# Performance work log

Hardware: AMD Instinct MI355X
Metric: run time of the kernel (lower is better)

Reference implementation:

```python
import jax, jax.numpy as jnp
import numpy as np

IN_FEATURES_LS = (8, 16, 32, 64, 128)
OUT_FEATURES = 512
MAX_FEAT = max(IN_FEATURES_LS)


def setup_inputs() -> dict:
    key = jax.random.key(0)
    k_x, k_idx, k_w, k_b = jax.random.split(key, 4)
    B, S = 16, 2048
    x = jax.random.normal(k_x, (B, S, MAX_FEAT), dtype=jnp.float32)
    # actual patch size per token: sample an index into in_features_ls
    idx = jax.random.randint(k_idx, (B, S), 0, len(IN_FEATURES_LS))
    in_feat_size = jnp.array(IN_FEATURES_LS, dtype=jnp.int64)[idx]
    weight = jax.random.normal(k_w, (len(IN_FEATURES_LS), OUT_FEATURES, MAX_FEAT), dtype=jnp.float32) * 0.05
    bias = jax.random.normal(k_b, (len(IN_FEATURES_LS), OUT_FEATURES), dtype=jnp.float32) * 0.05
    return {"x": x, "in_feat_size": in_feat_size, "weight": weight, "bias": bias}


def reference(x, in_feat_size, weight, bias):
    sizes = jnp.asarray(IN_FEATURES_LS)                       # [K]
    # mask padding columns of each expert's weight: [K, max_feat]
    feat_mask = (jnp.arange(MAX_FEAT)[None, :] < sizes[:, None]).astype(x.dtype)
    w = weight * feat_mask[:, None, :]                        # [K, out, max_feat]
    # all K projections computed unconditionally (faithful to original)
    y = jnp.einsum('bsi,koi->bsko', x, w) + bias              # [B, S, K, out]
    sel = (in_feat_size[..., None] == sizes).astype(x.dtype)  # [B, S, K] one-hot
    return jnp.einsum('bsko,bsk->bso', y, sel)                # [B, S, out]
```

## Files before the change

### kernel.cpp

```cpp
#include <hip/hip_runtime.h>

#define NEXP 5
#define MAXF 128
#define NOUT 512
#define NBMAX 256
#define PERMOFF (64 + NBMAX * NEXP)

typedef __attribute__((ext_vector_type(8))) short short8;
typedef __attribute__((ext_vector_type(4))) float floatx4;

__device__ __forceinline__ ushort f2bf(float f) {
    uint u = __float_as_uint(f);
    u += 0x7FFF + ((u >> 16) & 1);
    return (ushort)(u >> 16);
}


__global__ __launch_bounds__(256) void misl_prep(
    const int* __restrict__ feat, const float* __restrict__ w,
    int* __restrict__ ws, ushort* __restrict__ wb, int n, int nb) {
    if ((int)blockIdx.x < nb) {
        __shared__ int lcnt[NEXP];
        const int tid = threadIdx.x;
        if (tid < NEXP) lcnt[tid] = 0;
        __syncthreads();
        const int t = blockIdx.x * 256 + tid;
        if (t < n) { const int e = __ffs(feat[t]) - 4; atomicAdd(&lcnt[e], 1); }
        __syncthreads();
        if (tid < NEXP) ws[64 + blockIdx.x * NEXP + tid] = lcnt[tid];
    } else {
        const int idx = ((int)blockIdx.x - nb) * 256 + threadIdx.x;
        const int lane = idx & 63, nb16 = (idx >> 6) & 31;
        const int s = (idx >> 11) & 3, e = idx >> 13;
        if (e < NEXP) {
            const int ncol = nb16 * 16 + (lane & 15);
            const int k0 = s * 32 + (lane >> 4) * 8;
            const int K = 8 << e;
            const float* wr = w + ((size_t)e * NOUT + ncol) * MAXF + k0;
            short8 v;
            #pragma unroll
            for (int j = 0; j < 8; ++j)
                v[j] = (short)((k0 + j < K) ? f2bf(wr[j]) : (ushort)0);
            *(short8*)(wb + (size_t)idx * 8) = v;
        }
    }
}

__global__ __launch_bounds__(256) void misl_scatter(
    const int* __restrict__ feat, int* __restrict__ ws, int n, int nb) {
    __shared__ int ph[NBMAX * NEXP];
    __shared__ int lcnt[NEXP], lbase[NEXP], ltot[NEXP];
    const int tid = threadIdx.x;
    for (int i = tid; i < nb * NEXP; i += 256) ph[i] = ws[64 + i];
    if (tid < NEXP) lcnt[tid] = 0;
    __syncthreads();
    if (tid < NEXP) {
        int tot = 0, pre = 0;
        for (int bb = 0; bb < nb; ++bb) {
            if (bb == (int)blockIdx.x) pre = tot;
            tot += ph[bb * NEXP + tid];
        }
        ltot[tid] = tot; lbase[tid] = pre;
    }
    __syncthreads();
    if (tid < NEXP) {
        int seg = 0;
        for (int e = 0; e < tid; ++e) seg += ltot[e];
        lbase[tid] += seg;
        if (blockIdx.x == 0) { ws[tid] = ltot[tid]; ws[8 + tid] = seg; }
    }
    __syncthreads();
    const int t = blockIdx.x * 256 + tid;
    if (t < n) {
        const int e = __ffs(feat[t]) - 4;
        const int r = atomicAdd(&lcnt[e], 1);
        ws[PERMOFF + lbase[e] + r] = t;
    }
}

template <int NS>
__device__ __forceinline__ void mfma_group(
    const float* __restrict__ x, const ushort* __restrict__ wbe,
    const float* __restrict__ be, const int* __restrict__ ltok, int tcnt,
    int lane, int n_base, float* __restrict__ out) {
    const int m = lane & 15, q = lane >> 4;
    floatx4 acc[4];
    #pragma unroll
    for (int bi = 0; bi < 4; ++bi) {
        const float bv = be[n_base + bi * 16 + m];
        acc[bi] = floatx4{bv, bv, bv, bv};
    }
    const int tokA = ltok[m];
    const float* xr = x + (size_t)tokA * MAXF + q * 8;
    #pragma unroll
    for (int s = 0; s < NS; ++s) {
        const float4 xa = *(const float4*)(xr + s * 32);
        const float4 xb = *(const float4*)(xr + s * 32 + 4);
        short8 af;
        af[0] = (short)f2bf(xa.x); af[1] = (short)f2bf(xa.y);
        af[2] = (short)f2bf(xa.z); af[3] = (short)f2bf(xa.w);
        af[4] = (short)f2bf(xb.x); af[5] = (short)f2bf(xb.y);
        af[6] = (short)f2bf(xb.z); af[7] = (short)f2bf(xb.w);
        #pragma unroll
        for (int bi = 0; bi < 4; ++bi) {
            const short8 bf = *(const short8*)(
                wbe + ((size_t)(s * 32 + (n_base >> 4) + bi) * 64 + lane) * 8);
            acc[bi] = __builtin_amdgcn_mfma_f32_16x16x32_bf16(af, bf, acc[bi], 0, 0, 0);
        }
    }
    #pragma unroll
    for (int r = 0; r < 4; ++r) {
        const int mi = q * 4 + r;
        if (mi < tcnt) {
            const int tok = ltok[mi];
            float* orow = out + (size_t)tok * NOUT + n_base + m;
            #pragma unroll
            for (int bi = 0; bi < 4; ++bi) orow[bi * 16] = acc[bi][r];
        }
    }
}

__global__ __launch_bounds__(256) void misl_main(
    const float* __restrict__ x, const ushort* __restrict__ wb,
    const float* __restrict__ b, const int* __restrict__ ws,
    float* __restrict__ out) {
    const int g = blockIdx.x >> 1;
    const int half = blockIdx.x & 1;
    const int c[NEXP] = {ws[0], ws[1], ws[2], ws[3], ws[4]};
    const int sg[NEXP] = {ws[8], ws[9], ws[10], ws[11], ws[12]};

    int gb = 0, e = -1, lg = 0;
    #pragma unroll
    for (int j = 0; j < NEXP; ++j) {
        const int ee = 4 - j;
        const int ng = (c[ee] + 15) >> 4;
        if (e < 0 && g < gb + ng) { e = ee; lg = g - gb; }
        gb += ng;
    }
    if (e < 0) return;

    int tcnt = c[e] - lg * 16;
    if (tcnt > 16) tcnt = 16;

    __shared__ int ltok[16];
    if (threadIdx.x < 16) {
        const int ti = ((int)threadIdx.x < tcnt) ? (int)threadIdx.x : tcnt - 1;
        ltok[threadIdx.x] = ws[PERMOFF + sg[e] + lg * 16 + ti];
    }
    __syncthreads();

    const int lane = threadIdx.x & 63;
    const int wave = __builtin_amdgcn_readfirstlane(threadIdx.x >> 6);
    const int n_base = half * 256 + wave * 64;
    const ushort* wbe = wb + (size_t)e * 4 * 32 * 64 * 8;
    const float* be = b + e * NOUT;

    switch (e) {
        case 0: mfma_group<1>(x, wbe, be, ltok, tcnt, lane, n_base, out); break;
        case 1: mfma_group<1>(x, wbe, be, ltok, tcnt, lane, n_base, out); break;
        case 2: mfma_group<1>(x, wbe, be, ltok, tcnt, lane, n_base, out); break;
        case 3: mfma_group<2>(x, wbe, be, ltok, tcnt, lane, n_base, out); break;
        case 4: mfma_group<4>(x, wbe, be, ltok, tcnt, lane, n_base, out); break;
    }
}

extern "C" void kernel_launch(void* const* d_in, const int* in_sizes, int n_in,
                              void* d_out, int out_size, void* d_ws, size_t ws_size,
                              hipStream_t stream) {
    const float* x    = (const float*)d_in[0];
    const int*   feat = (const int*)d_in[1];
    const float* w    = (const float*)d_in[2];
    const float* b    = (const float*)d_in[3];
    float* out = (float*)d_out;
    int*   ws  = (int*)d_ws;

    const int n  = in_sizes[1];
    const int nb = (n + 255) / 256;

    const size_t wb_off = (((size_t)(PERMOFF + n)) * 4 + 255) & ~(size_t)255;
    ushort* wb = (ushort*)((char*)d_ws + wb_off);

    misl_prep<<<nb + 160, 256, 0, stream>>>(feat, w, ws, wb, n, nb);
    misl_scatter<<<nb, 256, 0, stream>>>(feat, ws, n, nb);
    misl_main<<<(n / 16 + NEXP) * 2, 256, 0, stream>>>(x, wb, b, ws, out);
}
```

Baseline: 107.0 us.

## Pre-convert x to bf16, reuse weight fragments across 64-token groups

Converts x to bf16 in a separate pre-pass fused with the scatter and weight-conversion kernel, and moves the histogram into its own small kernel. The main kernel now gives each block 64 tokens instead of 16, holds the weight fragments in registers and loops over four 16-token MFMA tiles. Token indices come straight from global memory, and a shuffle replaces the shared-memory token list and its barrier. This cuts repeated weight loads and per-block setup. In exchange it adds an extra full read and write of x in bf16 and uses more registers.

Result: faster. 100.0 us (-6.5%).

```diff
diff --git a/kernel.cpp b/kernel.cpp
--- a/kernel.cpp
+++ b/kernel.cpp
@@ -16,20 +16,53 @@
 }
 
 
-__global__ __launch_bounds__(256) void misl_prep(
-    const int* __restrict__ feat, const float* __restrict__ w,
-    int* __restrict__ ws, ushort* __restrict__ wb, int n, int nb) {
+__global__ __launch_bounds__(256) void misl_hist(
+    const int* __restrict__ feat, int* __restrict__ ws, int n) {
+    __shared__ int lcnt[NEXP];
+    const int tid = threadIdx.x;
+    if (tid < NEXP) lcnt[tid] = 0;
+    __syncthreads();
+    const int t = blockIdx.x * 256 + tid;
+    if (t < n) { const int e = __ffs(feat[t]) - 4; atomicAdd(&lcnt[e], 1); }
+    __syncthreads();
+    if (tid < NEXP) ws[64 + blockIdx.x * NEXP + tid] = lcnt[tid];
+}
+
+__global__ __launch_bounds__(256) void misl_rest(
+    const int* __restrict__ feat, const float* __restrict__ x,
+    const float* __restrict__ w, int* __restrict__ ws,
+    ushort* __restrict__ wb, ushort* __restrict__ xb, int n, int nb) {
+    const int tid = threadIdx.x;
     if ((int)blockIdx.x < nb) {
-        __shared__ int lcnt[NEXP];
-        const int tid = threadIdx.x;
+        __shared__ int ph[NBMAX * NEXP];
+        __shared__ int lcnt[NEXP], lbase[NEXP], ltot[NEXP];
+        for (int i = tid; i < nb * NEXP; i += 256) ph[i] = ws[64 + i];
         if (tid < NEXP) lcnt[tid] = 0;
         __syncthreads();
+        if (tid < NEXP) {
+            int tot = 0, pre = 0;
+            for (int bb = 0; bb < nb; ++bb) {
+                if (bb == (int)blockIdx.x) pre = tot;
+                tot += ph[bb * NEXP + tid];
+            }
+            ltot[tid] = tot; lbase[tid] = pre;
+        }
+        __syncthreads();
+        if (tid < NEXP) {
+            int seg = 0;
+            for (int e = 0; e < tid; ++e) seg += ltot[e];
+            lbase[tid] += seg;
+            if (blockIdx.x == 0) { ws[tid] = ltot[tid]; ws[8 + tid] = seg; }
+        }
+        __syncthreads();
         const int t = blockIdx.x * 256 + tid;
-        if (t < n) { const int e = __ffs(feat[t]) - 4; atomicAdd(&lcnt[e], 1); }
-        __syncthreads();
-        if (tid < NEXP) ws[64 + blockIdx.x * NEXP + tid] = lcnt[tid];
-    } else {
-        const int idx = ((int)blockIdx.x - nb) * 256 + threadIdx.x;
+        if (t < n) {
+            const int e = __ffs(feat[t]) - 4;
+            const int r = atomicAdd(&lcnt[e], 1);
+            ws[PERMOFF + lbase[e] + r] = t;
+        }
+    } else if ((int)blockIdx.x < nb + 160) {
+        const int idx = ((int)blockIdx.x - nb) * 256 + tid;
         const int lane = idx & 63, nb16 = (idx >> 6) & 31;
         const int s = (idx >> 11) & 3, e = idx >> 13;
         if (e < NEXP) {
@@ -43,85 +76,71 @@
                 v[j] = (short)((k0 + j < K) ? f2bf(wr[j]) : (ushort)0);
             *(short8*)(wb + (size_t)idx * 8) = v;
         }
-    }
-}
-
-__global__ __launch_bounds__(256) void misl_scatter(
-    const int* __restrict__ feat, int* __restrict__ ws, int n, int nb) {
-    __shared__ int ph[NBMAX * NEXP];
-    __shared__ int lcnt[NEXP], lbase[NEXP], ltot[NEXP];
-    const int tid = threadIdx.x;
-    for (int i = tid; i < nb * NEXP; i += 256) ph[i] = ws[64 + i];
-    if (tid < NEXP) lcnt[tid] = 0;
-    __syncthreads();
-    if (tid < NEXP) {
-        int tot = 0, pre = 0;
-        for (int bb = 0; bb < nb; ++bb) {
-            if (bb == (int)blockIdx.x) pre = tot;
-            tot += ph[bb * NEXP + tid];
-        }
-        ltot[tid] = tot; lbase[tid] = pre;
-    }
-    __syncthreads();
-    if (tid < NEXP) {
-        int seg = 0;
-        for (int e = 0; e < tid; ++e) seg += ltot[e];
-        lbase[tid] += seg;
-        if (blockIdx.x == 0) { ws[tid] = ltot[tid]; ws[8 + tid] = seg; }
-    }
-    __syncthreads();
-    const int t = blockIdx.x * 256 + tid;
-    if (t < n) {
-        const int e = __ffs(feat[t]) - 4;
-        const int r = atomicAdd(&lcnt[e], 1);
-        ws[PERMOFF + lbase[e] + r] = t;
+    } else {
+        const int idx = ((int)blockIdx.x - nb - 160) * 256 + tid;
+        if (idx < n * 16) {
+            const float4 a = *(const float4*)(x + (size_t)idx * 8);
+            const float4 c = *(const float4*)(x + (size_t)idx * 8 + 4);
+            short8 v;
+            v[0] = (short)f2bf(a.x); v[1] = (short)f2bf(a.y);
+            v[2] = (short)f2bf(a.z); v[3] = (short)f2bf(a.w);
+            v[4] = (short)f2bf(c.x); v[5] = (short)f2bf(c.y);
+            v[6] = (short)f2bf(c.z); v[7] = (short)f2bf(c.w);
+            *(short8*)(xb + (size_t)idx * 8) = v;
+        }
     }
 }
 
 template <int NS>
-__device__ __forceinline__ void mfma_group(
-    const float* __restrict__ x, const ushort* __restrict__ wbe,
-    const float* __restrict__ be, const int* __restrict__ ltok, int tcnt,
+__device__ __forceinline__ void mfma_run(
+    const ushort* __restrict__ xb, const ushort* __restrict__ wbe,
+    const float* __restrict__ be, const int* __restrict__ tokp, int rem,
     int lane, int n_base, float* __restrict__ out) {
     const int m = lane & 15, q = lane >> 4;
-    floatx4 acc[4];
+    const int nb16 = n_base >> 4;
+    short8 bf[NS][4];
     #pragma unroll
-    for (int bi = 0; bi < 4; ++bi) {
-        const float bv = be[n_base + bi * 16 + m];
-        acc[bi] = floatx4{bv, bv, bv, bv};
-    }
-    const int tokA = ltok[m];
-    const float* xr = x + (size_t)tokA * MAXF + q * 8;
+    for (int s = 0; s < NS; ++s)
+        #pragma unroll
+        for (int bi = 0; bi < 4; ++bi)
+            bf[s][bi] = *(const short8*)(wbe + ((size_t)((s * 32 + nb16 + bi)) * 64 + lane) * 8);
+    float bv[4];
     #pragma unroll
-    for (int s = 0; s < NS; ++s) {
-        const float4 xa = *(const float4*)(xr + s * 32);
-        const float4 xb = *(const float4*)(xr + s * 32 + 4);
-        short8 af;
-        af[0] = (short)f2bf(xa.x); af[1] = (short)f2bf(xa.y);
-        af[2] = (short)f2bf(xa.z); af[3] = (short)f2bf(xa.w);
-        af[4] = (short)f2bf(xb.x); af[5] = (short)f2bf(xb.y);
-        af[6] = (short)f2bf(xb.z); af[7] = (short)f2bf(xb.w);
-        #pragma unroll
-        for (int bi = 0; bi < 4; ++bi) {
-            const short8 bf = *(const short8*)(
-                wbe + ((size_t)(s * 32 + (n_base >> 4) + bi) * 64 + lane) * 8);
-            acc[bi] = __builtin_amdgcn_mfma_f32_16x16x32_bf16(af, bf, acc[bi], 0, 0, 0);
-        }
-    }
-    #pragma unroll
-    for (int r = 0; r < 4; ++r) {
-        const int mi = q * 4 + r;
-        if (mi < tcnt) {
-            const int tok = ltok[mi];
-            float* orow = out + (size_t)tok * NOUT + n_base + m;
+    for (int bi = 0; bi < 4; ++bi) bv[bi] = be[n_base + bi * 16 + m];
+
+    const int trips = (rem + 15) >> 4;
+    for (int g = 0; g < trips; ++g) {
+        const int base = g * 16;
+        const int lim = rem - base;
+        const int idx = (m < lim) ? m : lim - 1;
+        const int tokv = tokp[base + idx];
+        const ushort* xr = xb + (size_t)tokv * MAXF + q * 8;
+        floatx4 acc[4];
+        #pragma unroll
+        for (int bi = 0; bi < 4; ++bi)
+            acc[bi] = floatx4{bv[bi], bv[bi], bv[bi], bv[bi]};
+        #pragma unroll
+        for (int s = 0; s < NS; ++s) {
+            const short8 af = *(const short8*)(xr + s * 32);
             #pragma unroll
-            for (int bi = 0; bi < 4; ++bi) orow[bi * 16] = acc[bi][r];
+            for (int bi = 0; bi < 4; ++bi)
+                acc[bi] = __builtin_amdgcn_mfma_f32_16x16x32_bf16(af, bf[s][bi], acc[bi], 0, 0, 0);
+        }
+        #pragma unroll
+        for (int r = 0; r < 4; ++r) {
+            const int mi = q * 4 + r;
+            const int tr = __shfl(tokv, mi, 16);
+            if (mi < lim) {
+                float* orow = out + (size_t)tr * NOUT + n_base + m;
+                #pragma unroll
+                for (int bi = 0; bi < 4; ++bi) orow[bi * 16] = acc[bi][r];
+            }
         }
     }
 }
 
 __global__ __launch_bounds__(256) void misl_main(
-    const float* __restrict__ x, const ushort* __restrict__ wb,
+    const ushort* __restrict__ xb, const ushort* __restrict__ wb,
     const float* __restrict__ b, const int* __restrict__ ws,
     float* __restrict__ out) {
     const int g = blockIdx.x >> 1;
@@ -129,38 +148,31 @@
     const int c[NEXP] = {ws[0], ws[1], ws[2], ws[3], ws[4]};
     const int sg[NEXP] = {ws[8], ws[9], ws[10], ws[11], ws[12]};
 
-    int gb = 0, e = -1, lg = 0;
+    int gb = 0, e = -1, lgs = 0;
     #pragma unroll
     for (int j = 0; j < NEXP; ++j) {
         const int ee = 4 - j;
-        const int ng = (c[ee] + 15) >> 4;
-        if (e < 0 && g < gb + ng) { e = ee; lg = g - gb; }
+        const int ng = (c[ee] + 63) >> 6;
+        if (e < 0 && g < gb + ng) { e = ee; lgs = g - gb; }
         gb += ng;
     }
     if (e < 0) return;
 
-    int tcnt = c[e] - lg * 16;
-    if (tcnt > 16) tcnt = 16;
-
-    __shared__ int ltok[16];
-    if (threadIdx.x < 16) {
-        const int ti = ((int)threadIdx.x < tcnt) ? (int)threadIdx.x : tcnt - 1;
-        ltok[threadIdx.x] = ws[PERMOFF + sg[e] + lg * 16 + ti];
-    }
-    __syncthreads();
-
+    int rem = c[e] - lgs * 64;
+    if (rem > 64) rem = 64;
+    const int* tokp = ws + PERMOFF + sg[e] + lgs * 64;
     const int lane = threadIdx.x & 63;
-    const int wave = __builtin_amdgcn_readfirstlane(threadIdx.x >> 6);
+    const int wave = threadIdx.x >> 6;
     const int n_base = half * 256 + wave * 64;
     const ushort* wbe = wb + (size_t)e * 4 * 32 * 64 * 8;
     const float* be = b + e * NOUT;
 
     switch (e) {
-        case 0: mfma_group<1>(x, wbe, be, ltok, tcnt, lane, n_base, out); break;
-        case 1: mfma_group<1>(x, wbe, be, ltok, tcnt, lane, n_base, out); break;
-        case 2: mfma_group<1>(x, wbe, be, ltok, tcnt, lane, n_base, out); break;
-        case 3: mfma_group<2>(x, wbe, be, ltok, tcnt, lane, n_base, out); break;
-        case 4: mfma_group<4>(x, wbe, be, ltok, tcnt, lane, n_base, out); break;
+        case 0: mfma_run<1>(xb, wbe, be, tokp, rem, lane, n_base, out); break;
+        case 1: mfma_run<1>(xb, wbe, be, tokp, rem, lane, n_base, out); break;
+        case 2: mfma_run<1>(xb, wbe, be, tokp, rem, lane, n_base, out); break;
+        case 3: mfma_run<2>(xb, wbe, be, tokp, rem, lane, n_base, out); break;
+        case 4: mfma_run<4>(xb, wbe, be, tokp, rem, lane, n_base, out); break;
     }
 }
 
@@ -179,8 +191,11 @@
 
     const size_t wb_off = (((size_t)(PERMOFF + n)) * 4 + 255) & ~(size_t)255;
     ushort* wb = (ushort*)((char*)d_ws + wb_off);
-
-    misl_prep<<<nb + 160, 256, 0, stream>>>(feat, w, ws, wb, n, nb);
-    misl_scatter<<<nb, 256, 0, stream>>>(feat, ws, n, nb);
-    misl_main<<<(n / 16 + NEXP) * 2, 256, 0, stream>>>(x, wb, b, ws, out);
-}
+    const size_t xb_off = (wb_off + (size_t)NEXP * 4 * 32 * 64 * 8 * 2 + 255) & ~(size_t)255;
+    ushort* xb = (ushort*)((char*)d_ws + xb_off);
+
+    misl_hist<<<nb, 256, 0, stream>>>(feat, ws, n);
+    const int cvb = (n * 16 + 255) / 256;
+    misl_rest<<<nb + 160 + cvb, 256, 0, stream>>>(feat, x, w, ws, wb, xb, n, nb);
+    misl_main<<<((n + 63) / 64 + NEXP) * 2, 256, 0, stream>>>(xb, wb, b, ws, out);
+}
```
